# Performance work log

Hardware: AMD Instinct MI355X
Metric: run time of the kernel (lower is better)

The kernel has to match this reference:

```python
import jax, jax.numpy as jnp
import numpy as np
import math

C = 256
HEADS = 8
WS1 = (8, 8)
SS1 = (0, 0)
WS2 = (8, 8)
SS2 = (4, 4)
CPB_HIDDEN = 512


def _rel_pos_index(ws):
    coords = np.stack(np.meshgrid(np.arange(ws[0]), np.arange(ws[1]), indexing="ij")).reshape(2, -1)
    rel = (coords[:, :, None] - coords[:, None, :]).transpose(1, 2, 0).astype(np.int64)
    rel[..., 0] += ws[0] - 1
    rel[..., 1] += ws[1] - 1
    rel[..., 0] *= 2 * ws[1] - 1
    return rel.sum(-1).reshape(-1)


def _coords_table(ws):
    ch = np.arange(-(ws[0] - 1), ws[0], dtype=np.float32)
    cw = np.arange(-(ws[1] - 1), ws[1], dtype=np.float32)
    t = np.stack(np.meshgrid(ch, cw, indexing="ij"), axis=-1)
    t[..., 0] /= ws[0] - 1
    t[..., 1] /= ws[1] - 1
    t *= 8.0
    t = np.sign(t) * np.log2(np.abs(t) + 1.0) / 3.0
    return t.reshape(-1, 2)


def _swin_mask(pH, pW, ws, ss):
    # standard swin shifted-window attention mask, [num_windows, N, N]
    m = np.zeros((pH, pW), dtype=np.float32)
    cnt = 0.0
    hs = ((0, pH - ws[0]), (pH - ws[0], pH - ss[0]), (pH - ss[0], pH))
    wl = ((0, pW - ws[1]), (pW - ws[1], pW - ss[1]), (pW - ss[1], pW))
    for h0, h1 in hs:
        for w0, w1 in wl:
            m[h0:h1, w0:w1] = cnt
            cnt += 1.0
    m = m.reshape(pH // ws[0], ws[0], pW // ws[1], ws[1]).transpose(0, 2, 1, 3).reshape(-1, ws[0] * ws[1])
    diff = m[:, None, :] - m[:, :, None]
    return np.where(diff != 0.0, -100.0, 0.0).astype(np.float32)


def _swin_attn_v2(x, qkv_w, qkv_b, proj_w, proj_b, logit_scale, cpb_w1, cpb_b1, cpb_w2, ws, ss, num_heads):
    # torchvision ShiftedWindowAttentionV2 forward (dropout=0, eval)
    B, H, W, Cc = x.shape
    L = qkv_b.shape[0] // 3
    qkv_b = jnp.concatenate([qkv_b[:L], jnp.zeros_like(qkv_b[L:2 * L]), qkv_b[2 * L:]])  # v2 zeroes key bias
    pad_b = (ws[0] - H % ws[0]) % ws[0]
    pad_r = (ws[1] - W % ws[1]) % ws[1]
    x = jnp.pad(x, ((0, 0), (0, pad_b), (0, pad_r), (0, 0)))
    pH, pW = H + pad_b, W + pad_r
    s0 = 0 if ws[0] >= pH else ss[0]
    s1 = 0 if ws[1] >= pW else ss[1]
    shifted = (s0 > 0) or (s1 > 0)
    if shifted:
        x = jnp.roll(x, (-s0, -s1), axis=(1, 2))
    nH, nW = pH // ws[0], pW // ws[1]
    N = ws[0] * ws[1]
    xw = x.reshape(B, nH, ws[0], nW, ws[1], Cc).transpose(0, 1, 3, 2, 4, 5).reshape(B * nH * nW, N, Cc)
    qkv = (xw @ qkv_w.T + qkv_b).reshape(-1, N, 3, num_heads, Cc // num_heads).transpose(2, 0, 3, 1, 4)
    q, k, v = qkv[0], qkv[1], qkv[2]
    qn = q / jnp.maximum(jnp.linalg.norm(q, axis=-1, keepdims=True), 1e-12)
    kn = k / jnp.maximum(jnp.linalg.norm(k, axis=-1, keepdims=True), 1e-12)
    scale = jnp.exp(jnp.minimum(logit_scale, math.log(100.0)))  # [heads,1,1]
    attn = jnp.einsum("bhnd,bhmd->bhnm", qn, kn) * scale[None]
    # continuous relative position bias (v2)
    table = jnp.asarray(_coords_table(ws))
    bias_table = jax.nn.relu(table @ cpb_w1.T + cpb_b1) @ cpb_w2.T
    rpb = bias_table[_rel_pos_index(ws)].reshape(N, N, num_heads).transpose(2, 0, 1)
    attn = attn + 16.0 * jax.nn.sigmoid(rpb)[None]
    if shifted:
        mask = jnp.asarray(_swin_mask(pH, pW, ws, (s0, s1)))  # [nWin, N, N]
        attn = (attn.reshape(B, nH * nW, num_heads, N, N) + mask[None, :, None]).reshape(-1, num_heads, N, N)
    attn = jax.nn.softmax(attn, axis=-1)
    out = jnp.einsum("bhnm,bhmd->bhnd", attn, v).transpose(0, 2, 1, 3).reshape(-1, N, Cc)
    out = out @ proj_w.T + proj_b
    out = out.reshape(B, nH, nW, ws[0], ws[1], Cc).transpose(0, 1, 3, 2, 4, 5).reshape(B, pH, pW, Cc)
    if shifted:
        out = jnp.roll(out, (s0, s1), axis=(1, 2))
    return out[:, :H, :W, :]


def _make_params(keys):
    return {
        "qkv_w": jax.random.normal(keys[0], (3 * C, C), dtype=jnp.float32) * 0.02,
        "qkv_b": jax.random.normal(keys[1], (3 * C,), dtype=jnp.float32) * 0.02,
        "proj_w": jax.random.normal(keys[2], (C, C), dtype=jnp.float32) * 0.02,
        "proj_b": jax.random.normal(keys[3], (C,), dtype=jnp.float32) * 0.02,
        "logit_scale": jnp.full((HEADS, 1, 1), math.log(10.0), dtype=jnp.float32),
        "cpb_w1": jax.random.normal(keys[4], (CPB_HIDDEN, 2), dtype=jnp.float32) * 0.02,
        "cpb_b1": jnp.zeros((CPB_HIDDEN,), dtype=jnp.float32),
        "cpb_w2": jax.random.normal(keys[5], (HEADS, CPB_HIDDEN), dtype=jnp.float32) * 0.02,
    }


def setup_inputs() -> dict:
    key = jax.random.key(0)
    ks = jax.random.split(key, 13)
    d = {"src": jax.random.normal(ks[0], (4, 8, C, 64, 64), dtype=jnp.float32)}
    for pre, off in (("a1", 1), ("a2", 7)):
        for name, val in _make_params(ks[off:off + 6]).items():
            d[pre + "_" + name] = val
    return d


def reference(src, a1_qkv_w, a1_qkv_b, a1_proj_w, a1_proj_b, a1_logit_scale, a1_cpb_w1, a1_cpb_b1, a1_cpb_w2, a2_qkv_w, a2_qkv_b, a2_proj_w, a2_proj_b, a2_logit_scale, a2_cpb_w1, a2_cpb_b1, a2_cpb_w2):
    B, T, Cc, H, W = src.shape
    x = src.reshape(B * T, Cc, H, W).transpose(0, 2, 3, 1)  # [BT,H,W,C]
    x = x + _swin_attn_v2(x, a1_qkv_w, a1_qkv_b, a1_proj_w, a1_proj_b, a1_logit_scale, a1_cpb_w1, a1_cpb_b1, a1_cpb_w2, WS1, SS1, HEADS)
    x = x + _swin_attn_v2(x, a2_qkv_w, a2_qkv_b, a2_proj_w, a2_proj_b, a2_logit_scale, a2_cpb_w1, a2_cpb_b1, a2_cpb_w2, WS2, SS2, HEADS)
    return x.transpose(0, 3, 1, 2).reshape(src.shape)
```

## Files before the change

### kernel.cpp

```cpp
#include <hip/hip_runtime.h>


typedef short bf16x8 __attribute__((ext_vector_type(8)));
typedef float f32x4 __attribute__((ext_vector_type(4)));

__device__ __forceinline__ unsigned short f2bf(float f) {
    union { float f; unsigned int u; } v; v.f = f;
    return (unsigned short)((v.u + 0x7fffu + ((v.u >> 16) & 1u)) >> 16);
}
__device__ __forceinline__ float bf2f(unsigned short b) {
    union { unsigned int u; float f; } v; v.u = ((unsigned int)b) << 16;
    return v.f;
}
__device__ __forceinline__ f32x4 mfma_bf16(bf16x8 a, bf16x8 b, f32x4 c) {
    return __builtin_amdgcn_mfma_f32_16x16x32_bf16(a, b, c, 0, 0, 0);
}

__device__ __forceinline__ int region_of(int wh, int ww, int t) {
    int th = t >> 3, tw = t & 7;
    int rh = (wh == 7) ? ((th < 4) ? 1 : 2) : 0;
    int rw = (ww == 7) ? ((tw < 4) ? 1 : 2) : 0;
    return rh * 3 + rw;
}

__global__ __launch_bounds__(256) void k_setup(
    const float* __restrict__ qkvw1, const float* __restrict__ projw1,
    const float* __restrict__ qkvw2, const float* __restrict__ projw2,
    const float* __restrict__ w1a, const float* __restrict__ b1a, const float* __restrict__ w2a,
    const float* __restrict__ w1b, const float* __restrict__ b1b, const float* __restrict__ w2b,
    unsigned short* __restrict__ qw1, unsigned short* __restrict__ pw1,
    unsigned short* __restrict__ qw2, unsigned short* __restrict__ pw2,
    float* __restrict__ bt1, float* __restrict__ bt2)
{
    int b = blockIdx.x, t = threadIdx.x;
    if (b < 512) {
        int idx = b * 256 + t;
        #pragma unroll
        for (int r = 0; r < 4; r++) {
            int i = idx + r * 131072;
            if (i < 196608)        qw1[i]          = f2bf(qkvw1[i]);
            else if (i < 262144)   pw1[i - 196608] = f2bf(projw1[i - 196608]);
            else if (i < 458752)   qw2[i - 262144] = f2bf(qkvw2[i - 262144]);
            else                   pw2[i - 458752] = f2bf(projw2[i - 458752]);
        }
    } else {
        int a = b - 512;
        const float* w1 = a ? w1b : w1a;
        const float* b1 = a ? b1b : b1a;
        const float* w2 = a ? w2b : w2a;
        float* out = a ? bt2 : bt1;
        int k = t;
        if (k >= 225) return;
        int ih = k / 15, iw = k % 15;
        float v0 = (float)(ih - 7) / 7.0f * 8.0f;
        float v1 = (float)(iw - 7) / 7.0f * 8.0f;
        float t0 = (v0 >= 0.f ? 1.f : -1.f) * log2f(fabsf(v0) + 1.f) / 3.0f;
        float t1 = (v1 >= 0.f ? 1.f : -1.f) * log2f(fabsf(v1) + 1.f) / 3.0f;
        float acc[8] = {0.f, 0.f, 0.f, 0.f, 0.f, 0.f, 0.f, 0.f};
        for (int c = 0; c < 512; c++) {
            float hc = t0 * w1[2 * c] + t1 * w1[2 * c + 1] + b1[c];
            hc = fmaxf(hc, 0.f);
            #pragma unroll
            for (int h = 0; h < 8; h++) acc[h] += hc * w2[h * 512 + c];
        }
        #pragma unroll
        for (int h = 0; h < 8; h++) out[k * 8 + h] = 16.f / (1.f + expf(-acc[h]));
    }
}

__global__ __launch_bounds__(256) void t_in(const float* __restrict__ src, float* __restrict__ dst) {
    __shared__ float tile[32][33];
    int img = blockIdx.z, hw0 = blockIdx.x * 32, c0 = blockIdx.y * 32;
    int x = threadIdx.x & 31, y = threadIdx.x >> 5;
    #pragma unroll
    for (int k = 0; k < 4; k++)
        tile[y + k * 8][x] = src[((size_t)img * 256 + c0 + y + k * 8) * 4096 + hw0 + x];
    __syncthreads();
    #pragma unroll
    for (int k = 0; k < 4; k++)
        dst[((size_t)img * 4096 + hw0 + y + k * 8) * 256 + c0 + x] = tile[x][y + k * 8];
}

__global__ __launch_bounds__(256) void t_out(const float* __restrict__ src, float* __restrict__ dst) {
    __shared__ float tile[32][33];
    int img = blockIdx.z, hw0 = blockIdx.x * 32, c0 = blockIdx.y * 32;
    int x = threadIdx.x & 31, y = threadIdx.x >> 5;
    #pragma unroll
    for (int k = 0; k < 4; k++)
        tile[y + k * 8][x] = src[((size_t)img * 4096 + hw0 + y + k * 8) * 256 + c0 + x];
    __syncthreads();
    #pragma unroll
    for (int k = 0; k < 4; k++)
        dst[((size_t)img * 256 + c0 + y + k * 8) * 4096 + hw0 + x] = tile[x][y + k * 8];
}

__global__ __launch_bounds__(256, 2) void k_attn(
    const float* __restrict__ Xin,
    const unsigned short* __restrict__ Wq,
    const float* __restrict__ bq,
    const float* __restrict__ lsc,
    const float* __restrict__ btab,
    unsigned short* __restrict__ AO,
    int shift, int masked)
{
    __shared__ __align__(16) unsigned short sX[64 * 264];
    __shared__ __align__(16) unsigned short sQKV[64 * 200];
    __shared__ __align__(16) unsigned short sP[64 * 72];
    __shared__ __align__(16) unsigned short sVt[64 * 72];
    __shared__ float sInv[4 * 64];

    const int tid = threadIdx.x;
    const int wv = tid >> 6, lane = tid & 63, quad = lane >> 4, nn = lane & 15;
    const int win = blockIdx.x;
    const int bt = win >> 6, wh = (win >> 3) & 7, ww = win & 7;
    const f32x4 zero4 = {0.f, 0.f, 0.f, 0.f};

    {
        int tok = tid >> 2, part = tid & 3;
        int h = (wh * 8 + (tok >> 3) + shift) & 63;
        int w = (ww * 8 + (tok & 7) + shift) & 63;
        const float* srcp = Xin + ((size_t)(bt * 4096 + h * 64 + w)) * 256 + part * 64;
        unsigned short* dstp = sX + tok * 264 + part * 64;
        #pragma unroll
        for (int c = 0; c < 64; c += 4) {
            float4 v = *(const float4*)(srcp + c);
            unsigned int p0 = (unsigned int)f2bf(v.x) | ((unsigned int)f2bf(v.y) << 16);
            unsigned int p1 = (unsigned int)f2bf(v.z) | ((unsigned int)f2bf(v.w) << 16);
            uint2 o; o.x = p0; o.y = p1;
            *(uint2*)(dstp + c) = o;
        }
    }
    __syncthreads();

    for (int p = 0; p < 4; p++) {
        f32x4 acc[4][3];
        #pragma unroll
        for (int rt = 0; rt < 4; rt++)
            #pragma unroll
            for (int c = 0; c < 3; c++) acc[rt][c] = zero4;

        int wrow[3], cbase[3], kindv[3];
        #pragma unroll
        for (int c = 0; c < 3; c++) {
            int ct = wv * 3 + c;
            int sec = ct >> 1;
            int kind = sec >> 1;
            int head = 2 * p + (sec & 1);
            wrow[c] = kind * 256 + head * 32 + (ct & 1) * 16 + nn;
            cbase[c] = ct * 16 + nn;
            kindv[c] = kind;
        }
        #pragma unroll
        for (int ks = 0; ks < 8; ks++) {
            bf16x8 a[4], b[3];
            #pragma unroll
            for (int rt = 0; rt < 4; rt++)
                a[rt] = *(const bf16x8*)(sX + (rt * 16 + nn) * 264 + ks * 32 + quad * 8);
            #pragma unroll
            for (int c = 0; c < 3; c++)
                b[c] = *(const bf16x8*)(Wq + (size_t)wrow[c] * 256 + ks * 32 + quad * 8);
            #pragma unroll
            for (int rt = 0; rt < 4; rt++)
                #pragma unroll
                for (int c = 0; c < 3; c++)
                    acc[rt][c] = mfma_bf16(a[rt], b[c], acc[rt][c]);
        }
        #pragma unroll
        for (int c = 0; c < 3; c++) {
            float bias = (kindv[c] == 1) ? 0.f : bq[wrow[c]];
            #pragma unroll
            for (int rt = 0; rt < 4; rt++)
                #pragma unroll
                for (int r = 0; r < 4; r++) {
                    int tokr = rt * 16 + quad * 4 + r;
                    sQKV[tokr * 200 + cbase[c]] = f2bf(acc[rt][c][r] + bias);
                }
        }
        __syncthreads();

        {
            int t = tid & 63, which = tid >> 6;
            const unsigned short* row = sQKV + t * 200 + which * 32;
            float ss = 0.f;
            #pragma unroll
            for (int cc = 0; cc < 32; cc++) { float v = bf2f(row[cc]); ss += v * v; }
            sInv[which * 64 + t] = 1.f / fmaxf(sqrtf(ss), 1e-12f);
            #pragma unroll
            for (int dd = 0; dd < 16; dd++) {
                int d = which * 16 + dd;
                sVt[d * 72 + t] = sQKV[t * 200 + 128 + d];
            }
        }
        __syncthreads();

        for (int hh = 0; hh < 2; hh++) {
            const int head = 2 * p + hh;
            const float scale = __expf(fminf(lsc[head], 4.605170185988092f));

            bf16x8 aq = *(const bf16x8*)(sQKV + (wv * 16 + nn) * 200 + hh * 32 + quad * 8);
            f32x4 S[4];
            #pragma unroll
            for (int ct = 0; ct < 4; ct++) {
                bf16x8 bk = *(const bf16x8*)(sQKV + (ct * 16 + nn) * 200 + 64 + hh * 32 + quad * 8);
                S[ct] = mfma_bf16(aq, bk, zero4);
            }

            const float* invq = sInv + hh * 64;
            const float* invk = sInv + (2 + hh) * 64;
            const int i_base = wv * 16 + quad * 4;
            float rowm[4] = {-3.0e38f, -3.0e38f, -3.0e38f, -3.0e38f};
            int ri[4];
            #pragma unroll
            for (int r = 0; r < 4; r++) ri[r] = masked ? region_of(wh, ww, i_base + r) : 0;

            #pragma unroll
            for (int ct = 0; ct < 4; ct++) {
                int j = ct * 16 + nn;
                float ivk = invk[j];
                int rj = masked ? region_of(wh, ww, j) : 0;
                #pragma unroll
                for (int r = 0; r < 4; r++) {
                    int i = i_base + r;
                    float v = S[ct][r] * invq[i] * ivk * scale;
                    int rel = ((i >> 3) - (j >> 3) + 7) * 15 + ((i & 7) - (j & 7) + 7);
                    v += btab[rel * 8 + head];
                    if (masked && (ri[r] != rj)) v += -100.f;
                    S[ct][r] = v;
                    rowm[r] = fmaxf(rowm[r], v);
                }
            }
            #pragma unroll
            for (int r = 0; r < 4; r++) {
                float m = rowm[r];
                m = fmaxf(m, __shfl_xor(m, 1));
                m = fmaxf(m, __shfl_xor(m, 2));
                m = fmaxf(m, __shfl_xor(m, 4));
                m = fmaxf(m, __shfl_xor(m, 8));
                rowm[r] = m;
            }
            float rsum[4] = {0.f, 0.f, 0.f, 0.f};
            #pragma unroll
            for (int ct = 0; ct < 4; ct++)
                #pragma unroll
                for (int r = 0; r < 4; r++) {
                    float e = __expf(S[ct][r] - rowm[r]);
                    S[ct][r] = e;
                    rsum[r] += e;
                }
            #pragma unroll
            for (int r = 0; r < 4; r++) {
                float s = rsum[r];
                s += __shfl_xor(s, 1);
                s += __shfl_xor(s, 2);
                s += __shfl_xor(s, 4);
                s += __shfl_xor(s, 8);
                rsum[r] = 1.f / s;
            }
            #pragma unroll
            for (int ct = 0; ct < 4; ct++)
                #pragma unroll
                for (int r = 0; r < 4; r++)
                    sP[(i_base + r) * 72 + ct * 16 + nn] = f2bf(S[ct][r] * rsum[r]);

            bf16x8 ap0 = *(const bf16x8*)(sP + (wv * 16 + nn) * 72 + quad * 8);
            bf16x8 ap1 = *(const bf16x8*)(sP + (wv * 16 + nn) * 72 + 32 + quad * 8);
            #pragma unroll
            for (int ct2 = 0; ct2 < 2; ct2++) {
                bf16x8 bv0 = *(const bf16x8*)(sVt + (hh * 32 + ct2 * 16 + nn) * 72 + quad * 8);
                bf16x8 bv1 = *(const bf16x8*)(sVt + (hh * 32 + ct2 * 16 + nn) * 72 + 32 + quad * 8);
                f32x4 O = mfma_bf16(ap0, bv0, zero4);
                O = mfma_bf16(ap1, bv1, O);
                #pragma unroll
                for (int r = 0; r < 4; r++) {
                    int tokr = i_base + r;
                    AO[((size_t)win * 64 + tokr) * 256 + head * 32 + ct2 * 16 + nn] = f2bf(O[r]);
                }
            }
        }
        __syncthreads();
    }
}

__global__ __launch_bounds__(256, 4) void k_proj(
    const unsigned short* __restrict__ AO,
    const unsigned short* __restrict__ Wp,
    const float* __restrict__ bp,
    const float* __restrict__ Xres,
    float* __restrict__ Xout,
    int shift)
{
    __shared__ __align__(16) unsigned short sO[64 * 264];
    const int tid = threadIdx.x;
    const int wv = tid >> 6, lane = tid & 63, quad = lane >> 4, nn = lane & 15;
    const int win = blockIdx.x;
    const int bt = win >> 6, wh = (win >> 3) & 7, ww = win & 7;
    const f32x4 zero4 = {0.f, 0.f, 0.f, 0.f};

    {
        int tok = tid >> 2, part = tid & 3;
        const unsigned short* srcp = AO + ((size_t)win * 64 + tok) * 256 + part * 64;
        unsigned short* dstp = sO + tok * 264 + part * 64;
        #pragma unroll
        for (int c = 0; c < 64; c += 8)
            *(uint4*)(dstp + c) = *(const uint4*)(srcp + c);
    }
    __syncthreads();

    f32x4 acc[4][4];
    #pragma unroll
    for (int rt = 0; rt < 4; rt++)
        #pragma unroll
        for (int c = 0; c < 4; c++) acc[rt][c] = zero4;

    int wrow[4];
    #pragma unroll
    for (int c = 0; c < 4; c++) wrow[c] = (wv * 4 + c) * 16 + nn;

    #pragma unroll
    for (int ks = 0; ks < 8; ks++) {
        bf16x8 a[4], b[4];
        #pragma unroll
        for (int rt = 0; rt < 4; rt++)
            a[rt] = *(const bf16x8*)(sO + (rt * 16 + nn) * 264 + ks * 32 + quad * 8);
        #pragma unroll
        for (int c = 0; c < 4; c++)
            b[c] = *(const bf16x8*)(Wp + (size_t)wrow[c] * 256 + ks * 32 + quad * 8);
        #pragma unroll
        for (int rt = 0; rt < 4; rt++)
            #pragma unroll
            for (int c = 0; c < 4; c++)
                acc[rt][c] = mfma_bf16(a[rt], b[c], acc[rt][c]);
    }

    #pragma unroll
    for (int c = 0; c < 4; c++) {
        int chan = wrow[c];
        float bias = bp[chan];
        #pragma unroll
        for (int rt = 0; rt < 4; rt++)
            #pragma unroll
            for (int r = 0; r < 4; r++) {
                int tok = rt * 16 + quad * 4 + r;
                int h = (wh * 8 + (tok >> 3) + shift) & 63;
                int w = (ww * 8 + (tok & 7) + shift) & 63;
                size_t idx = ((size_t)(bt * 4096 + h * 64 + w)) * 256 + chan;
                Xout[idx] = acc[rt][c][r] + bias + Xres[idx];
            }
    }
}

extern "C" void kernel_launch(void* const* d_in, const int* in_sizes, int n_in,
                              void* d_out, int out_size, void* d_ws, size_t ws_size,
                              hipStream_t stream) {
    (void)in_sizes; (void)n_in; (void)out_size; (void)ws_size;

    const float* src        = (const float*)d_in[0];
    const float* a1_qkv_w   = (const float*)d_in[1];
    const float* a1_qkv_b   = (const float*)d_in[2];
    const float* a1_proj_w  = (const float*)d_in[3];
    const float* a1_proj_b  = (const float*)d_in[4];
    const float* a1_ls      = (const float*)d_in[5];
    const float* a1_w1      = (const float*)d_in[6];
    const float* a1_b1      = (const float*)d_in[7];
    const float* a1_w2      = (const float*)d_in[8];
    const float* a2_qkv_w   = (const float*)d_in[9];
    const float* a2_qkv_b   = (const float*)d_in[10];
    const float* a2_proj_w  = (const float*)d_in[11];
    const float* a2_proj_b  = (const float*)d_in[12];
    const float* a2_ls      = (const float*)d_in[13];
    const float* a2_w1      = (const float*)d_in[14];
    const float* a2_b1      = (const float*)d_in[15];
    const float* a2_w2      = (const float*)d_in[16];

    char* ws = (char*)d_ws;
    const size_t SZ_X = 134217728;
    float* X0 = (float*)(ws);
    float* X1 = (float*)(ws + SZ_X);
    unsigned short* AO  = (unsigned short*)(ws + 2 * SZ_X);
    unsigned short* qw1 = (unsigned short*)(ws + 2 * SZ_X + 67108864);
    unsigned short* qw2 = qw1 + 196608;
    unsigned short* pw1 = qw2 + 196608;
    unsigned short* pw2 = pw1 + 65536;
    float* bt1 = (float*)(pw2 + 65536);
    float* bt2 = bt1 + 1800;

    k_setup<<<514, 256, 0, stream>>>(a1_qkv_w, a1_proj_w, a2_qkv_w, a2_proj_w,
                                     a1_w1, a1_b1, a1_w2, a2_w1, a2_b1, a2_w2,
                                     qw1, pw1, qw2, pw2, bt1, bt2);
    t_in<<<dim3(128, 8, 32), 256, 0, stream>>>(src, X0);

    k_attn<<<2048, 256, 0, stream>>>(X0, qw1, a1_qkv_b, a1_ls, bt1, AO, 0, 0);
    k_proj<<<2048, 256, 0, stream>>>(AO, pw1, a1_proj_b, X0, X1, 0);
    k_attn<<<2048, 256, 0, stream>>>(X1, qw2, a2_qkv_b, a2_ls, bt2, AO, 4, 1);
    k_proj<<<2048, 256, 0, stream>>>(AO, pw2, a2_proj_b, X1, X0, 4);

    t_out<<<dim3(128, 8, 32), 256, 0, stream>>>(X0, (float*)d_out);
}
```

Measured before the change: 1.081 ms.

## Widen attention blocks to 512 threads and precompute dense bias tables

Doubles k_attn to 8 waves so each wave owns a 32-row slice of the QKV GEMM and one head in the attention phase, with both heads of a pair processed in parallel using separate P buffers. L2 norms and the V transpose now come straight from the GEMM accumulators via shuffles, which removes the separate normalize/transpose pass and one barrier. A new k_expand kernel materializes the per-head 64x64 relative-position bias so the inner loop does a direct load instead of index arithmetic plus a gather. In exchange, each wave re-reads the weight rows from global memory, and the larger block may limit occupancy.

```diff
diff --git a/kernel.cpp b/kernel.cpp
--- a/kernel.cpp
+++ b/kernel.cpp
@@ -7,10 +7,6 @@
 __device__ __forceinline__ unsigned short f2bf(float f) {
     union { float f; unsigned int u; } v; v.f = f;
     return (unsigned short)((v.u + 0x7fffu + ((v.u >> 16) & 1u)) >> 16);
-}
-__device__ __forceinline__ float bf2f(unsigned short b) {
-    union { unsigned int u; float f; } v; v.u = ((unsigned int)b) << 16;
-    return v.f;
 }
 __device__ __forceinline__ f32x4 mfma_bf16(bf16x8 a, bf16x8 b, f32x4 c) {
     return __builtin_amdgcn_mfma_f32_16x16x32_bf16(a, b, c, 0, 0, 0);
@@ -68,6 +64,20 @@
     }
 }
 
+__global__ __launch_bounds__(256) void k_expand(
+    const float* __restrict__ bt1, const float* __restrict__ bt2,
+    float* __restrict__ BT1, float* __restrict__ BT2)
+{
+    int idx = blockIdx.x * 256 + threadIdx.x;
+    int a = idx >> 15, rest = idx & 32767;
+    int head = rest >> 12, ij = rest & 4095;
+    int i = ij >> 6, j = ij & 63;
+    int rel = ((i >> 3) - (j >> 3) + 7) * 15 + ((i & 7) - (j & 7) + 7);
+    const float* src = a ? bt2 : bt1;
+    float* dst = a ? BT2 : BT1;
+    dst[head * 4096 + ij] = src[rel * 8 + head];
+}
+
 __global__ __launch_bounds__(256) void t_in(const float* __restrict__ src, float* __restrict__ dst) {
     __shared__ float tile[32][33];
     int img = blockIdx.z, hw0 = blockIdx.x * 32, c0 = blockIdx.y * 32;
@@ -94,18 +104,18 @@
         dst[((size_t)img * 256 + c0 + y + k * 8) * 4096 + hw0 + x] = tile[x][y + k * 8];
 }
 
-__global__ __launch_bounds__(256, 2) void k_attn(
+__global__ __launch_bounds__(512, 4) void k_attn(
     const float* __restrict__ Xin,
     const unsigned short* __restrict__ Wq,
     const float* __restrict__ bq,
     const float* __restrict__ lsc,
-    const float* __restrict__ btab,
+    const float* __restrict__ BT,
     unsigned short* __restrict__ AO,
     int shift, int masked)
 {
     __shared__ __align__(16) unsigned short sX[64 * 264];
-    __shared__ __align__(16) unsigned short sQKV[64 * 200];
-    __shared__ __align__(16) unsigned short sP[64 * 72];
+    __shared__ __align__(16) unsigned short sQK[64 * 136];
+    __shared__ __align__(16) unsigned short sP[2 * 64 * 72];
     __shared__ __align__(16) unsigned short sVt[64 * 72];
     __shared__ float sInv[4 * 64];
 
@@ -116,13 +126,13 @@
     const f32x4 zero4 = {0.f, 0.f, 0.f, 0.f};
 
     {
-        int tok = tid >> 2, part = tid & 3;
+        int tok = tid >> 3, part = tid & 7;
         int h = (wh * 8 + (tok >> 3) + shift) & 63;
         int w = (ww * 8 + (tok & 7) + shift) & 63;
-        const float* srcp = Xin + ((size_t)(bt * 4096 + h * 64 + w)) * 256 + part * 64;
-        unsigned short* dstp = sX + tok * 264 + part * 64;
-        #pragma unroll
-        for (int c = 0; c < 64; c += 4) {
+        const float* srcp = Xin + ((size_t)(bt * 4096 + h * 64 + w)) * 256 + part * 32;
+        unsigned short* dstp = sX + tok * 264 + part * 32;
+        #pragma unroll
+        for (int c = 0; c < 32; c += 4) {
             float4 v = *(const float4*)(srcp + c);
             unsigned int p0 = (unsigned int)f2bf(v.x) | ((unsigned int)f2bf(v.y) << 16);
             unsigned int p1 = (unsigned int)f2bf(v.z) | ((unsigned int)f2bf(v.w) << 16);
@@ -132,87 +142,93 @@
     }
     __syncthreads();
 
+    const int h2 = wv & 1, s = wv >> 1;
+    const int rb = h2 * 32;
+    const int kindq = (s < 2);
+    const int g = wv >> 1, hh = wv & 1;
+
     for (int p = 0; p < 4; p++) {
-        f32x4 acc[4][3];
-        #pragma unroll
-        for (int rt = 0; rt < 4; rt++)
-            #pragma unroll
-            for (int c = 0; c < 3; c++) acc[rt][c] = zero4;
-
-        int wrow[3], cbase[3], kindv[3];
-        #pragma unroll
-        for (int c = 0; c < 3; c++) {
-            int ct = wv * 3 + c;
-            int sec = ct >> 1;
-            int kind = sec >> 1;
-            int head = 2 * p + (sec & 1);
-            wrow[c] = kind * 256 + head * 32 + (ct & 1) * 16 + nn;
-            cbase[c] = ct * 16 + nn;
-            kindv[c] = kind;
-        }
+        int wrow0 = (s >> 1) * 256 + (2 * p + (s & 1)) * 32 + nn;
+        int wrow1 = wrow0 + 16;
+        int wrowv = 512 + p * 64 + s * 16 + nn;
+
+        f32x4 acc00 = zero4, acc01 = zero4, acc0v = zero4;
+        f32x4 acc10 = zero4, acc11 = zero4, acc1v = zero4;
         #pragma unroll
         for (int ks = 0; ks < 8; ks++) {
-            bf16x8 a[4], b[3];
-            #pragma unroll
-            for (int rt = 0; rt < 4; rt++)
-                a[rt] = *(const bf16x8*)(sX + (rt * 16 + nn) * 264 + ks * 32 + quad * 8);
-            #pragma unroll
-            for (int c = 0; c < 3; c++)
-                b[c] = *(const bf16x8*)(Wq + (size_t)wrow[c] * 256 + ks * 32 + quad * 8);
-            #pragma unroll
-            for (int rt = 0; rt < 4; rt++)
-                #pragma unroll
-                for (int c = 0; c < 3; c++)
-                    acc[rt][c] = mfma_bf16(a[rt], b[c], acc[rt][c]);
-        }
-        #pragma unroll
-        for (int c = 0; c < 3; c++) {
-            float bias = (kindv[c] == 1) ? 0.f : bq[wrow[c]];
-            #pragma unroll
-            for (int rt = 0; rt < 4; rt++)
+            bf16x8 a0 = *(const bf16x8*)(sX + (rb + nn) * 264 + ks * 32 + quad * 8);
+            bf16x8 a1 = *(const bf16x8*)(sX + (rb + 16 + nn) * 264 + ks * 32 + quad * 8);
+            bf16x8 b0 = *(const bf16x8*)(Wq + (size_t)wrow0 * 256 + ks * 32 + quad * 8);
+            bf16x8 b1 = *(const bf16x8*)(Wq + (size_t)wrow1 * 256 + ks * 32 + quad * 8);
+            bf16x8 bv = *(const bf16x8*)(Wq + (size_t)wrowv * 256 + ks * 32 + quad * 8);
+            acc00 = mfma_bf16(a0, b0, acc00);
+            acc10 = mfma_bf16(a1, b0, acc10);
+            acc01 = mfma_bf16(a0, b1, acc01);
+            acc11 = mfma_bf16(a1, b1, acc11);
+            acc0v = mfma_bf16(a0, bv, acc0v);
+            acc1v = mfma_bf16(a1, bv, acc1v);
+        }
+
+        __syncthreads();
+
+        {
+            float bia0 = kindq ? bq[wrow0] : 0.f;
+            float bia1 = kindq ? bq[wrow1] : 0.f;
+            float biav = bq[wrowv];
+            #pragma unroll
+            for (int rt = 0; rt < 2; rt++) {
+                const f32x4 A0 = rt ? acc10 : acc00;
+                const f32x4 A1 = rt ? acc11 : acc01;
+                const f32x4 AV = rt ? acc1v : acc0v;
+                int tb = rb + rt * 16 + quad * 4;
+                float ss[4];
                 #pragma unroll
                 for (int r = 0; r < 4; r++) {
-                    int tokr = rt * 16 + quad * 4 + r;
-                    sQKV[tokr * 200 + cbase[c]] = f2bf(acc[rt][c][r] + bias);
+                    float v0 = A0[r] + bia0;
+                    float v1 = A1[r] + bia1;
+                    float vv = AV[r] + biav;
+                    sQK[(tb + r) * 136 + s * 32 + nn]      = f2bf(v0);
+                    sQK[(tb + r) * 136 + s * 32 + 16 + nn] = f2bf(v1);
+                    sVt[(s * 16 + nn) * 72 + tb + r]       = f2bf(vv);
+                    ss[r] = v0 * v0 + v1 * v1;
                 }
+                #pragma unroll
+                for (int r = 0; r < 4; r++) {
+                    ss[r] += __shfl_xor(ss[r], 1);
+                    ss[r] += __shfl_xor(ss[r], 2);
+                    ss[r] += __shfl_xor(ss[r], 4);
+                    ss[r] += __shfl_xor(ss[r], 8);
+                }
+                if (nn < 4)
+                    sInv[s * 64 + tb + nn] = 1.f / fmaxf(sqrtf(ss[nn]), 1e-12f);
+            }
         }
         __syncthreads();
 
         {
-            int t = tid & 63, which = tid >> 6;
-            const unsigned short* row = sQKV + t * 200 + which * 32;
-            float ss = 0.f;
-            #pragma unroll
-            for (int cc = 0; cc < 32; cc++) { float v = bf2f(row[cc]); ss += v * v; }
-            sInv[which * 64 + t] = 1.f / fmaxf(sqrtf(ss), 1e-12f);
-            #pragma unroll
-            for (int dd = 0; dd < 16; dd++) {
-                int d = which * 16 + dd;
-                sVt[d * 72 + t] = sQKV[t * 200 + 128 + d];
-            }
-        }
-        __syncthreads();
-
-        for (int hh = 0; hh < 2; hh++) {
             const int head = 2 * p + hh;
             const float scale = __expf(fminf(lsc[head], 4.605170185988092f));
 
-            bf16x8 aq = *(const bf16x8*)(sQKV + (wv * 16 + nn) * 200 + hh * 32 + quad * 8);
+            bf16x8 aq = *(const bf16x8*)(sQK + (g * 16 + nn) * 136 + hh * 32 + quad * 8);
             f32x4 S[4];
             #pragma unroll
             for (int ct = 0; ct < 4; ct++) {
-                bf16x8 bk = *(const bf16x8*)(sQKV + (ct * 16 + nn) * 200 + 64 + hh * 32 + quad * 8);
+                bf16x8 bk = *(const bf16x8*)(sQK + (ct * 16 + nn) * 136 + 64 + hh * 32 + quad * 8);
                 S[ct] = mfma_bf16(aq, bk, zero4);
             }
 
-            const float* invq = sInv + hh * 64;
+            const int i_base = g * 16 + quad * 4;
+            float invq[4];
+            int ri[4];
+            #pragma unroll
+            for (int r = 0; r < 4; r++) {
+                invq[r] = sInv[hh * 64 + i_base + r];
+                ri[r] = masked ? region_of(wh, ww, i_base + r) : 0;
+            }
+            const float* btp = BT + head * 4096;
             const float* invk = sInv + (2 + hh) * 64;
-            const int i_base = wv * 16 + quad * 4;
+
             float rowm[4] = {-3.0e38f, -3.0e38f, -3.0e38f, -3.0e38f};
-            int ri[4];
-            #pragma unroll
-            for (int r = 0; r < 4; r++) ri[r] = masked ? region_of(wh, ww, i_base + r) : 0;
-
             #pragma unroll
             for (int ct = 0; ct < 4; ct++) {
                 int j = ct * 16 + nn;
@@ -220,10 +236,7 @@
                 int rj = masked ? region_of(wh, ww, j) : 0;
                 #pragma unroll
                 for (int r = 0; r < 4; r++) {
-                    int i = i_base + r;
-                    float v = S[ct][r] * invq[i] * ivk * scale;
-                    int rel = ((i >> 3) - (j >> 3) + 7) * 15 + ((i & 7) - (j & 7) + 7);
-                    v += btab[rel * 8 + head];
+                    float v = S[ct][r] * invq[r] * ivk * scale + btp[(i_base + r) * 64 + j];
                     if (masked && (ri[r] != rj)) v += -100.f;
                     S[ct][r] = v;
                     rowm[r] = fmaxf(rowm[r], v);
@@ -249,21 +262,22 @@
                 }
             #pragma unroll
             for (int r = 0; r < 4; r++) {
-                float s = rsum[r];
-                s += __shfl_xor(s, 1);
-                s += __shfl_xor(s, 2);
-                s += __shfl_xor(s, 4);
-                s += __shfl_xor(s, 8);
-                rsum[r] = 1.f / s;
-            }
+                float sm = rsum[r];
+                sm += __shfl_xor(sm, 1);
+                sm += __shfl_xor(sm, 2);
+                sm += __shfl_xor(sm, 4);
+                sm += __shfl_xor(sm, 8);
+                rsum[r] = 1.f / sm;
+            }
+            unsigned short* sPh = sP + hh * 4608;
             #pragma unroll
             for (int ct = 0; ct < 4; ct++)
                 #pragma unroll
                 for (int r = 0; r < 4; r++)
-                    sP[(i_base + r) * 72 + ct * 16 + nn] = f2bf(S[ct][r] * rsum[r]);
-
-            bf16x8 ap0 = *(const bf16x8*)(sP + (wv * 16 + nn) * 72 + quad * 8);
-            bf16x8 ap1 = *(const bf16x8*)(sP + (wv * 16 + nn) * 72 + 32 + quad * 8);
+                    sPh[(i_base + r) * 72 + ct * 16 + nn] = f2bf(S[ct][r] * rsum[r]);
+
+            bf16x8 ap0 = *(const bf16x8*)(sPh + (g * 16 + nn) * 72 + quad * 8);
+            bf16x8 ap1 = *(const bf16x8*)(sPh + (g * 16 + nn) * 72 + 32 + quad * 8);
             #pragma unroll
             for (int ct2 = 0; ct2 < 2; ct2++) {
                 bf16x8 bv0 = *(const bf16x8*)(sVt + (hh * 32 + ct2 * 16 + nn) * 72 + quad * 8);
@@ -271,13 +285,10 @@
                 f32x4 O = mfma_bf16(ap0, bv0, zero4);
                 O = mfma_bf16(ap1, bv1, O);
                 #pragma unroll
-                for (int r = 0; r < 4; r++) {
-                    int tokr = i_base + r;
-                    AO[((size_t)win * 64 + tokr) * 256 + head * 32 + ct2 * 16 + nn] = f2bf(O[r]);
-                }
-            }
-        }
-        __syncthreads();
+                for (int r = 0; r < 4; r++)
+                    AO[((size_t)win * 64 + i_base + r) * 256 + head * 32 + ct2 * 16 + nn] = f2bf(O[r]);
+            }
+        }
     }
 }
 
@@ -383,15 +394,18 @@
     unsigned short* pw2 = pw1 + 65536;
     float* bt1 = (float*)(pw2 + 65536);
     float* bt2 = bt1 + 1800;
+    float* BT1 = bt2 + 1800;
+    float* BT2 = BT1 + 32768;
 
     k_setup<<<514, 256, 0, stream>>>(a1_qkv_w, a1_proj_w, a2_qkv_w, a2_proj_w,
                                      a1_w1, a1_b1, a1_w2, a2_w1, a2_b1, a2_w2,
                                      qw1, pw1, qw2, pw2, bt1, bt2);
+    k_expand<<<256, 256, 0, stream>>>(bt1, bt2, BT1, BT2);
     t_in<<<dim3(128, 8, 32), 256, 0, stream>>>(src, X0);
 
-    k_attn<<<2048, 256, 0, stream>>>(X0, qw1, a1_qkv_b, a1_ls, bt1, AO, 0, 0);
+    k_attn<<<2048, 512, 0, stream>>>(X0, qw1, a1_qkv_b, a1_ls, BT1, AO, 0, 0);
     k_proj<<<2048, 256, 0, stream>>>(AO, pw1, a1_proj_b, X0, X1, 0);
-    k_attn<<<2048, 256, 0, stream>>>(X1, qw2, a2_qkv_b, a2_ls, bt2, AO, 4, 1);
+    k_attn<<<2048, 512, 0, stream>>>(X1, qw2, a2_qkv_b, a2_ls, BT2, AO, 4, 1);
     k_proj<<<2048, 256, 0, stream>>>(AO, pw2, a2_proj_b, X1, X0, 4);
 
     t_out<<<dim3(128, 8, 32), 256, 0, stream>>>(X0, (float*)d_out);
```

New measurement: 1.141 ms. +5.5%, slower.
